# Kernel optimization log

Measured on AMD Instinct MI355X. Metric: run time of the kernel, lower is better.

The kernel has to match this reference:

```python
import jax, jax.numpy as jnp
import numpy as np

EPS = 1e-6
T = 10.0
STEPS = 3
BN_EPS = 1e-5

def _normalize(x, axis):
    n = jnp.sqrt(jnp.sum(x * x, axis=axis, keepdims=True))
    return x / jnp.maximum(n, EPS)

def _vq_step(X, D):
    # X: (B, d, n), D: (B, d, r)
    Dn = _normalize(D, 1)
    Xn = _normalize(X, 1)
    cos = jnp.einsum('bdr,bdn->brn', Dn, Xn)          # (B, r, n)
    C = jax.nn.softmax(cos / T, axis=1)               # softmax over r
    XCt = jnp.einsum('bdn,brn->bdr', X, C)            # (B, d, r)
    sums = jnp.maximum(jnp.sum(C, axis=2), EPS)       # (B, r)
    D2 = _normalize(XCt / sums[:, None, :], 1)
    Xbar = jnp.einsum('bdr,brn->bdn', D2, C)
    return D2, C, Xbar

def _ham_vq(X, D0):
    # K-1 steps without gradient tracking, final step with grad through X only
    Xs = jax.lax.stop_gradient(X)
    def body(D, _):
        D, _, _ = _vq_step(Xs, D)
        return D, None
    D, _ = jax.lax.scan(body, _normalize(D0, 1), None, length=STEPS - 1)
    D = jax.lax.stop_gradient(D)
    _, _, Xbar = _vq_step(X, D)
    return Xbar

def _conv1x1(x, w, b=None):
    y = jnp.einsum('oc,bchw->bohw', w, x)
    if b is not None:
        y = y + b[None, :, None, None]
    return y

def _bn(x, gamma, beta, mean, var):
    inv = gamma / jnp.sqrt(var + BN_EPS)
    return x * inv[None, :, None, None] + (beta - mean * inv)[None, :, None, None]


def setup_inputs() -> dict:
    key = jax.random.key(0)
    ks = jax.random.split(key, 16)
    B, Cin, H, W = 8, 512, 64, 64
    d_mid, r = 512, 64
    out_ch = 2 * d_mid  # dual
    sc = 0.02
    inp = {
        'z': jax.random.normal(ks[0], (B, Cin, H, W), jnp.float32),
        'lower_w': jax.random.normal(ks[1], (out_ch, Cin), jnp.float32) * sc,
        'lower_b': jnp.zeros((out_ch,), jnp.float32),
        'Dinit_s': jax.random.uniform(ks[2], (B, d_mid, r), jnp.float32),
        'Dinit_c': jax.random.uniform(ks[3], (B, d_mid, r), jnp.float32),
        'cheese_w': jax.random.normal(ks[4], (out_ch, out_ch), jnp.float32) * sc,
        'ch_gamma': jnp.ones((out_ch,), jnp.float32),
        'ch_beta': jnp.zeros((out_ch,), jnp.float32),
        'ch_mean': jax.random.normal(ks[5], (out_ch,), jnp.float32) * 0.1,
        'ch_var': jax.random.uniform(ks[6], (out_ch,), jnp.float32) + 0.5,
        'upper_w': jax.random.normal(ks[7], (Cin, out_ch), jnp.float32) * sc,
        'upper_b': jnp.zeros((Cin,), jnp.float32),
        'h_gamma': jnp.ones((Cin,), jnp.float32),
        'h_beta': jnp.zeros((Cin,), jnp.float32),
        'h_mean': jax.random.normal(ks[8], (Cin,), jnp.float32) * 0.1,
        'h_var': jax.random.uniform(ks[9], (Cin,), jnp.float32) + 0.5,
        'coef_ham': jnp.array(1.0, jnp.float32),
        'coef_shortcut': jnp.array(1.0, jnp.float32),
    }
    return inp


def reference(z, lower_w, lower_b, Dinit_s, Dinit_c, cheese_w,
              ch_gamma, ch_beta, ch_mean, ch_var, upper_w, upper_b,
              h_gamma, h_beta, h_mean, h_var, coef_ham, coef_shortcut):
    B, Cin, H, W = z.shape
    identity = z
    # lower: conv1x1 + relu
    y = jax.nn.relu(_conv1x1(z, lower_w, lower_b))       # (B, 2*d_mid, H, W)
    d_mid = y.shape[1] // 2
    y1, y2 = y[:, :d_mid], y[:, d_mid:]
    n = H * W
    # spatial ham
    Xs = y1.reshape(B, d_mid, n)
    y1 = _ham_vq(Xs, Dinit_s).reshape(B, d_mid, H, W)
    # channel ham (same (B, d, n) flattening; HamMD requires dim1 == d_mid)
    Xc = y2.reshape(B, d_mid, n)
    y2 = _ham_vq(Xc, Dinit_c).reshape(B, d_mid, H, W)
    y = jnp.concatenate([y1, y2], axis=1)
    # cheese: conv1x1(no bias) + BN + relu
    y = jax.nn.relu(_bn(_conv1x1(y, cheese_w), ch_gamma, ch_beta, ch_mean, ch_var))
    # upper conv1x1 + BN
    h = _bn(_conv1x1(y, upper_w, upper_b), h_gamma, h_beta, h_mean, h_var)
    out = coef_ham * h + coef_shortcut * identity
    return jax.nn.relu(out)
```

## Files before the change

### kernel.cpp

```cpp
#include <hip/hip_runtime.h>
#include <hip/hip_bf16.h>

typedef __bf16 bf16_t;
typedef __bf16 bf16x4 __attribute__((ext_vector_type(4)));
typedef __bf16 bf16x8 __attribute__((ext_vector_type(8)));
typedef float  f32x4  __attribute__((ext_vector_type(4)));

#define HEPS 1e-6f

__device__ __forceinline__ void gload16(const bf16_t* g, bf16_t* l) {
    __builtin_amdgcn_global_load_lds(
        (const __attribute__((address_space(1))) unsigned int*)(g),
        (__attribute__((address_space(3))) unsigned int*)(l),
        16, 0, 0);
}

__global__ void setup_k(const float* __restrict__ wl, bf16_t* __restrict__ dwl,
                        const float* __restrict__ wc, bf16_t* __restrict__ dwc,
                        const float* __restrict__ wu, bf16_t* __restrict__ dwu,
                        const float* __restrict__ Ds, const float* __restrict__ Dc,
                        bf16_t* __restrict__ Dt,
                        const float* __restrict__ chg, const float* __restrict__ chb,
                        const float* __restrict__ chm, const float* __restrict__ chv,
                        const float* __restrict__ hg, const float* __restrict__ hb,
                        const float* __restrict__ hm, const float* __restrict__ hv,
                        const float* __restrict__ ub, const float* __restrict__ cham,
                        float* __restrict__ chA, float* __restrict__ chB,
                        float* __restrict__ hA2, float* __restrict__ hB2) {
    int bid = blockIdx.x;
    int tid = threadIdx.x;
    if (bid < 8192) {
        int i = bid * 256 + tid;
        if (i < 524288) dwl[i] = (bf16_t)wl[i];
        else if (i < 1572864) { int k = i - 524288; dwc[k] = (bf16_t)wc[k]; }
        else { int k = i - 1572864; dwu[k] = (bf16_t)wu[k]; }
    } else if (bid < 10240) {
        int b2 = bid - 8192;
        int bs = b2 >> 7;
        int idx = (b2 & 127) * 256 + tid;
        int b = bs >> 1;
        const float* src = ((bs & 1) ? Dc : Ds) + (size_t)b * 512 * 64;
        int r = idx & 63, d = idx >> 6;
        Dt[(size_t)bs * 64 * 512 + (size_t)r * 512 + d] = (bf16_t)src[d * 64 + r];
    } else {
        int i = (bid - 10240) * 256 + tid;
        if (i < 1024) {
            float inv = chg[i] * rsqrtf(chv[i] + 1e-5f);
            chA[i] = inv;
            chB[i] = chb[i] - chm[i] * inv;
        }
        if (i < 512) {
            float inv = hg[i] * rsqrtf(hv[i] + 1e-5f);
            float cA = cham[0];
            hA2[i] = cA * inv;
            hB2[i] = cA * (fmaf(ub[i], inv, hb[i]) - hm[i] * inv);
        }
    }
}

__global__ void tz_k(const float* __restrict__ z, bf16_t* __restrict__ Zt,
                     bf16_t* __restrict__ zb) {
    __shared__ bf16_t t[64][68];
    int b = blockIdx.z, kt = blockIdx.y, nt = blockIdx.x;
    const size_t boff = ((size_t)b * 512 + kt * 64) * 4096 + nt * 64;
    const float* src = z + boff;
    bf16_t* zbo = zb + boff;
    int tid = threadIdx.x;
    int kr = tid >> 4;
    int nc = (tid & 15) * 4;
    #pragma unroll
    for (int it = 0; it < 4; ++it) {
        int k = kr + it * 16;
        float4 v = *(const float4*)&src[(size_t)k * 4096 + nc];
        bf16x4 o;
        o[0] = (bf16_t)v.x; o[1] = (bf16_t)v.y; o[2] = (bf16_t)v.z; o[3] = (bf16_t)v.w;
        t[nc + 0][k] = o[0]; t[nc + 1][k] = o[1];
        t[nc + 2][k] = o[2]; t[nc + 3][k] = o[3];
        *(bf16x4*)&zbo[(size_t)k * 4096 + nc] = o;
    }
    __syncthreads();
    bf16_t* dst = Zt + ((size_t)b * 4096 + nt * 64) * 512 + kt * 64;
    int nr = tid >> 4;
    int kc = (tid & 15) * 4;
    #pragma unroll
    for (int it = 0; it < 4; ++it) {
        int n = nr + it * 16;
        bf16x4 o;
        #pragma unroll
        for (int c = 0; c < 4; ++c) o[c] = t[n][kc + c];
        *(bf16x4*)&dst[(size_t)n * 512 + kc] = o;
    }
}

__global__ void dnorm_k(const bf16_t* __restrict__ Dt, float* __restrict__ dinv) {
    int gw = (blockIdx.x * 256 + threadIdx.x) >> 6;
    int lane = threadIdx.x & 63;
    bf16x8 v = *(const bf16x8*)(Dt + (size_t)gw * 512 + lane * 8);
    float s = 0.f;
    #pragma unroll
    for (int e = 0; e < 8; ++e) { float f = (float)v[e]; s += f * f; }
    #pragma unroll
    for (int off = 32; off > 0; off >>= 1) s += __shfl_xor(s, off);
    if (lane == 0) dinv[gw] = 1.0f / fmaxf(sqrtf(s), HEPS);
}

__global__ void reduce_k(const float* __restrict__ P, bf16_t* __restrict__ Dt,
                         float* __restrict__ dinv) {
    int bsr = blockIdx.x;
    int bs = bsr >> 6, r = bsr & 63;
    int lane = threadIdx.x;
    const float* base = P + ((size_t)(bs * 8) * 64 + r) * 512 + lane * 8;
    float s[8] = {0.f, 0.f, 0.f, 0.f, 0.f, 0.f, 0.f, 0.f};
    #pragma unroll
    for (int kc = 0; kc < 8; ++kc) {
        const float* p = base + (size_t)kc * 64 * 512;
        float4 u = *(const float4*)p;
        float4 w = *(const float4*)(p + 4);
        s[0] += u.x; s[1] += u.y; s[2] += u.z; s[3] += u.w;
        s[4] += w.x; s[5] += w.y; s[6] += w.z; s[7] += w.w;
    }
    bf16x8 o;
    float sq = 0.f;
    #pragma unroll
    for (int e = 0; e < 8; ++e) { sq += s[e] * s[e]; o[e] = (bf16_t)s[e]; }
    *(bf16x8*)&Dt[(size_t)bsr * 512 + lane * 8] = o;
    #pragma unroll
    for (int off = 32; off > 0; off >>= 1) sq += __shfl_xor(sq, off);
    if (lane == 0) dinv[bsr] = 1.0f / fmaxf(sqrtf(sq), HEPS);
}

template<int BM, int BN, int WAVES_M, int WAVES_N, int EPI, int ORDER>
__launch_bounds__(256)
__global__ void g2(const bf16_t* __restrict__ Ag, const bf16_t* __restrict__ Bg,
                   void* __restrict__ Cg, void* __restrict__ C2g,
                   const int M, const int N, const int K,
                   const int ldA, const int ldB, const int ldC,
                   const long aStride, const long bStride,
                   const long cStride, const long c2Stride,
                   const float* __restrict__ p0, const float* __restrict__ p1,
                   const float* __restrict__ scal,
                   const void* __restrict__ shortcut, const long sStride)
{
    constexpr int WM = BM / WAVES_M, WN = BN / WAVES_N;
    constexpr int FM = WM / 16, FN = WN / 16;
    constexpr int ASEG = BM / 64, BSEG = BN / 64;
    constexpr int LPT = ASEG + BSEG;

    __shared__ __align__(64) bf16_t SH[3 * (BM + BN) * 32];
    __shared__ float dl[64];
    bf16_t* Al = SH;
    bf16_t* Bl = SH + 3 * BM * 32;

    const int tid = threadIdx.x;
    const int wave = tid >> 6, lane = tid & 63;
    const int l15 = lane & 15, q = lane >> 4;
    const int lrow = lane >> 2, lcol = (lane & 3) * 8;

    const int gx = gridDim.x, gy = gridDim.y;
    const int per = gx * gy;
    const int nwg = per * gridDim.z;
    const int g = blockIdx.z * per + blockIdx.y * gx + blockIdx.x;
    const int qq = nwg >> 3, rr = nwg & 7;
    const int xcd = g & 7, jj = g >> 3;
    const int w = (xcd < rr ? xcd * (qq + 1) : rr * (qq + 1) + (xcd - rr) * qq) + jj;
    const int bz = w / per;
    const int rem = w - bz * per;
    int bx, by;
    if constexpr (ORDER == 0) { by = rem / gx; bx = rem - by * gx; }
    else                      { bx = rem / gy; by = rem - bx * gy; }

    int bs = bz, exA = 0, exB = 0;
    if constexpr (EPI == 5) { bs = bz >> 3; exA = exB = (bz & 7) * 512; }
    if constexpr (EPI == 7) { exA = (bz & 1) * 512; }

    const int n0 = bx * BN;
    const int m0 = by * BM;
    const int wm0 = (wave / WAVES_N) * WM;
    const int wn0 = (wave % WAVES_N) * WN;

    const bf16_t* Ab;
    const bf16_t* Bb;
    if constexpr (EPI == 6) {
        Ab = Ag + (size_t)(bz >> 1) * (size_t)aStride + (size_t)(bz & 1) * 512;
        Bb = Bg + (size_t)bz * (size_t)bStride;
    } else {
        Ab = Ag + (size_t)bs * (size_t)aStride + exA;
        Bb = Bg + (size_t)bs * (size_t)bStride + exB;
    }

    if constexpr (EPI == 6) { if (tid < 64) dl[tid] = p0[bz * 64 + tid]; }

    auto stage = [&](int buf, int k0) {
        #pragma unroll
        for (int t = 0; t < ASEG; ++t) {
            int seg = wave * ASEG + t;
            gload16(Ab + (size_t)(m0 + seg * 16 + lrow) * ldA + k0 + lcol,
                    &Al[buf * BM * 32 + seg * 512]);
        }
        #pragma unroll
        for (int t = 0; t < BSEG; ++t) {
            int seg = wave * BSEG + t;
            gload16(Bb + (size_t)(n0 + seg * 16 + lrow) * ldB + k0 + lcol,
                    &Bl[buf * BN * 32 + seg * 512]);
        }
    };

    f32x4 acc[FM][FN];
    #pragma unroll
    for (int i = 0; i < FM; ++i)
        #pragma unroll
        for (int j = 0; j < FN; ++j)
            #pragma unroll
            for (int e = 0; e < 4; ++e) acc[i][j][e] = 0.f;

    float xsq[FM];
    #pragma unroll
    for (int i = 0; i < FM; ++i) xsq[i] = 0.f;

    const int nK = K / 32;
    stage(0, 0);
    if (nK > 1) stage(1, 32);

    for (int t = 0; t < nK; ++t) {
        const int cur = t % 3;

        if (t < nK - 1) asm volatile("s_waitcnt vmcnt(%0)" :: "i"(LPT) : "memory");
        else            asm volatile("s_waitcnt vmcnt(0)" ::: "memory");
        asm volatile("s_barrier" ::: "memory");
        __builtin_amdgcn_sched_barrier(0);

        if (t + 2 < nK) stage((t + 2) % 3, (t + 2) * 32);

        bf16x8 af[FM], bfm[FN];
        #pragma unroll
        for (int i = 0; i < FM; ++i)
            af[i] = *(const bf16x8*)&Al[cur * BM * 32 + (wm0 + 16 * i + l15) * 32 + 8 * q];
        #pragma unroll
        for (int j = 0; j < FN; ++j)
            bfm[j] = *(const bf16x8*)&Bl[cur * BN * 32 + (wn0 + 16 * j + l15) * 32 + 8 * q];

        if constexpr (EPI == 6) {
            #pragma unroll
            for (int i = 0; i < FM; ++i)
                #pragma unroll
                for (int e = 0; e < 8; ++e) {
                    float f = (float)af[i][e];
                    xsq[i] = fmaf(f, f, xsq[i]);
                }
        }

        __builtin_amdgcn_s_setprio(1);
        #pragma unroll
        for (int i = 0; i < FM; ++i)
            #pragma unroll
            for (int j = 0; j < FN; ++j)
                acc[i][j] = __builtin_amdgcn_mfma_f32_16x16x32_bf16(af[i], bfm[j], acc[i][j], 0, 0, 0);
        __builtin_amdgcn_s_setprio(0);
    }

    int rowB[FM];
    #pragma unroll
    for (int i = 0; i < FM; ++i) rowB[i] = m0 + wm0 + 16 * i + 4 * q;
    const int colBase = n0 + wn0;

    if constexpr (EPI == 2) {
        bf16_t* O = (bf16_t*)Cg + (size_t)bz * (size_t)cStride;
        #pragma unroll
        for (int j = 0; j < FN; ++j) {
            int col = colBase + 16 * j + l15;
            float a = p0[col], b = p1[col];
            #pragma unroll
            for (int i = 0; i < FM; ++i) {
                int rb = rowB[i];
                #pragma unroll
                for (int e = 0; e < 4; ++e) {
                    float v = fmaxf(fmaf(acc[i][j][e], a, b), 0.f);
                    O[(size_t)(rb + e) * ldC + col] = (bf16_t)v;
                }
            }
        }
    } else if constexpr (EPI == 3) {
        constexpr int SPAD = BN + 4;
        constexpr int V = (BM * BN) / 2048;
        float* O = (float*)Cg + (size_t)bz * (size_t)cStride;
        const bf16_t* scg = (const bf16_t*)shortcut + (size_t)bz * (size_t)sStride;
        bf16_t* SP = SH;
        float cB = scal[0];
        __syncthreads();
        #pragma unroll
        for (int v = 0; v < V; ++v) {
            int flat = (tid * V + v) * 8;
            int row = flat / BN, col = flat % BN;
            *(bf16x8*)&SP[row * SPAD + col] =
                *(const bf16x8*)&scg[(size_t)(m0 + row) * ldC + n0 + col];
        }
        __syncthreads();
        #pragma unroll
        for (int i = 0; i < FM; ++i) {
            int rl = wm0 + 16 * i + 4 * q;
            #pragma unroll
            for (int e = 0; e < 4; ++e) {
                int row = m0 + rl + e;
                float a = p0[row], b = p1[row];
                #pragma unroll
                for (int j = 0; j < FN; ++j) {
                    int cl = wn0 + 16 * j + l15;
                    float v = fmaf(acc[i][j][e], a, b)
                            + cB * (float)SP[(rl + e) * SPAD + cl];
                    O[(size_t)row * ldC + n0 + cl] = fmaxf(v, 0.f);
                }
            }
        }
    } else if constexpr (EPI == 5) {
        float* O = (float*)Cg + (size_t)bz * (size_t)cStride;
        #pragma unroll
        for (int i = 0; i < FM; ++i) {
            int rb = rowB[i];
            #pragma unroll
            for (int j = 0; j < FN; ++j) {
                int col = colBase + 16 * j + l15;
                *(f32x4*)&O[(size_t)col * ldC + rb] = acc[i][j];
            }
        }
    } else if constexpr (EPI == 6) {
        bf16_t* Cc = (bf16_t*)Cg  + (size_t)bz * (size_t)cStride;
        bf16_t* Ct = (bf16_t*)C2g + (size_t)(bz >> 1) * (size_t)c2Stride;
        const int hoff = (bz & 1) * 64;
        const bool doCt = (C2g != nullptr);
        float xs[FM];
        #pragma unroll
        for (int i = 0; i < FM; ++i) {
            float s2 = xsq[i];
            s2 += __shfl_xor(s2, 16);
            s2 += __shfl_xor(s2, 32);
            xs[i] = s2;
        }
        float di[FN];
        #pragma unroll
        for (int j = 0; j < FN; ++j) di[j] = dl[16 * j + l15];
        #pragma unroll
        for (int i = 0; i < FM; ++i) {
            int rb = rowB[i];
            bf16x4 tj[FN];
            #pragma unroll
            for (int e = 0; e < 4; ++e) {
                float s2row = __shfl(xs[i], 4 * q + e);
                float xi = 1.0f / (10.0f * fmaxf(sqrtf(s2row), HEPS));
                float v[FN];
                float mx = -1e30f;
                #pragma unroll
                for (int j = 0; j < FN; ++j) {
                    v[j] = acc[i][j][e] * di[j] * xi;
                    mx = fmaxf(mx, v[j]);
                }
                mx = fmaxf(mx, __shfl_xor(mx, 1));
                mx = fmaxf(mx, __shfl_xor(mx, 2));
                mx = fmaxf(mx, __shfl_xor(mx, 4));
                mx = fmaxf(mx, __shfl_xor(mx, 8));
                float sm = 0.f;
                #pragma unroll
                for (int j = 0; j < FN; ++j) { v[j] = __expf(v[j] - mx); sm += v[j]; }
                sm += __shfl_xor(sm, 1);
                sm += __shfl_xor(sm, 2);
                sm += __shfl_xor(sm, 4);
                sm += __shfl_xor(sm, 8);
                float rs = 1.0f / sm;
                #pragma unroll
                for (int j = 0; j < FN; ++j) {
                    float p = v[j] * rs;
                    tj[j][e] = (bf16_t)p;
                    if (doCt) Ct[(size_t)(rb + e) * 128 + hoff + 16 * j + l15] = (bf16_t)p;
                }
            }
            #pragma unroll
            for (int j = 0; j < FN; ++j)
                *(bf16x4*)&Cc[(size_t)(16 * j + l15) * ldC + rb] = tj[j];
        }
    } else if constexpr (EPI == 7) {
        bf16_t* O = (bf16_t*)Cg + (size_t)(bz >> 1) * (size_t)cStride;
        const int hoff = (bz & 1) * 64;
        #pragma unroll
        for (int j = 0; j < FN; ++j) {
            int col = colBase + 16 * j + l15;
            float di = p0[bz * 64 + col];
            #pragma unroll
            for (int i = 0; i < FM; ++i) {
                int rb = rowB[i];
                #pragma unroll
                for (int e = 0; e < 4; ++e)
                    O[(size_t)(rb + e) * 128 + hoff + col] = (bf16_t)(acc[i][j][e] * di);
            }
        }
    } else if constexpr (EPI == 8) {
        bf16_t* O  = (bf16_t*)Cg  + (size_t)bz * (size_t)cStride;
        bf16_t* O2 = (bf16_t*)C2g + (size_t)bz * (size_t)c2Stride;
        #pragma unroll
        for (int j = 0; j < FN; ++j) {
            int col = colBase + 16 * j + l15;
            float bias = p0[col];
            #pragma unroll
            for (int i = 0; i < FM; ++i) {
                int rb = rowB[i];
                bf16x4 t;
                #pragma unroll
                for (int e = 0; e < 4; ++e) {
                    float v = fmaxf(acc[i][j][e] + bias, 0.f);
                    t[e] = (bf16_t)v;
                    O[(size_t)(rb + e) * ldC + col] = t[e];
                }
                *(bf16x4*)&O2[(size_t)col * 4096 + rb] = t;
            }
        }
    }
}


extern "C" void kernel_launch(void* const* d_in, const int* in_sizes, int n_in,
                              void* d_out, int out_size, void* d_ws, size_t ws_size,
                              hipStream_t stream) {
    const float* z        = (const float*)d_in[0];
    const float* lower_w  = (const float*)d_in[1];
    const float* lower_b  = (const float*)d_in[2];
    const float* Dinit_s  = (const float*)d_in[3];
    const float* Dinit_c  = (const float*)d_in[4];
    const float* cheese_w = (const float*)d_in[5];
    const float* ch_gamma = (const float*)d_in[6];
    const float* ch_beta  = (const float*)d_in[7];
    const float* ch_mean  = (const float*)d_in[8];
    const float* ch_var   = (const float*)d_in[9];
    const float* upper_w  = (const float*)d_in[10];
    const float* upper_b  = (const float*)d_in[11];
    const float* h_gamma  = (const float*)d_in[12];
    const float* h_beta   = (const float*)d_in[13];
    const float* h_mean   = (const float*)d_in[14];
    const float* h_var    = (const float*)d_in[15];
    const float* coef_ham = (const float*)d_in[16];
    const float* coef_sc  = (const float*)d_in[17];

    char* ws = (char*)d_ws;
    size_t off = 0;
    auto alloc = [&](size_t bytes) -> void* {
        void* p = ws + off;
        off += (bytes + 255) & ~(size_t)255;
        return p;
    };

    bf16_t* Wl   = (bf16_t*)alloc((size_t)1024 * 512 * 2);
    bf16_t* Wc   = (bf16_t*)alloc((size_t)1024 * 1024 * 2);
    bf16_t* Wu   = (bf16_t*)alloc((size_t)512 * 1024 * 2);
    float*  chA  = (float*) alloc(1024 * 4);
    float*  chB  = (float*) alloc(1024 * 4);
    float*  hA2  = (float*) alloc(512 * 4);
    float*  hB2  = (float*) alloc(512 * 4);
    float*  dinv = (float*) alloc(1024 * 4);
    bf16_t* Xbf  = (bf16_t*)alloc((size_t)8 * 1024 * 4096 * 2);
    bf16_t* Xt   = (bf16_t*)alloc((size_t)8 * 4096 * 1024 * 2);
    bf16_t* Zt   = (bf16_t*)alloc((size_t)8 * 4096 * 512 * 2);
    bf16_t* zb   = (bf16_t*)alloc((size_t)8 * 512 * 4096 * 2);
    bf16_t* Cb   = (bf16_t*)alloc((size_t)16 * 64 * 4096 * 2);
    bf16_t* Ct2  = (bf16_t*)alloc((size_t)8 * 4096 * 128 * 2);
    float*  P    = (float*) alloc((size_t)128 * 64 * 512 * 4);
    bf16_t* Dta  = (bf16_t*)alloc((size_t)16 * 64 * 512 * 2);
    bf16_t* Dtb  = (bf16_t*)alloc((size_t)16 * 64 * 512 * 2);
    bf16_t* Eb   = (bf16_t*)alloc((size_t)8 * 1024 * 128 * 2);
    bf16_t* Ycht = Xbf;

    dim3 blk(256);

    setup_k<<<10244, blk, 0, stream>>>(lower_w, Wl, cheese_w, Wc, upper_w, Wu,
                                       Dinit_s, Dinit_c, Dta,
                                       ch_gamma, ch_beta, ch_mean, ch_var,
                                       h_gamma, h_beta, h_mean, h_var,
                                       upper_b, coef_ham, chA, chB, hA2, hB2);
    tz_k<<<dim3(64, 8, 8), blk, 0, stream>>>(z, Zt, zb);

    g2<128, 64, 2, 2, 8, 0><<<dim3(16, 32, 8), blk, 0, stream>>>(
        Zt, Wl, (void*)Xt, (void*)Xbf, 4096, 1024, 512,
        512, 512, 1024,
        (long)4096 * 512, 0L, (long)4096 * 1024, (long)1024 * 4096,
        lower_b, nullptr, nullptr, nullptr, 0L);

    dnorm_k<<<256, blk, 0, stream>>>(Dta, dinv);

    bf16_t* cur = Dta;
    bf16_t* nxt = Dtb;
    for (int t = 0; t < 3; ++t) {
        g2<128, 64, 4, 1, 6, 0><<<dim3(1, 32, 16), blk, 0, stream>>>(
            Xt, cur, (void*)Cb, (t == 2) ? (void*)Ct2 : nullptr, 4096, 64, 512,
            1024, 512, 4096,
            (long)4096 * 1024, (long)64 * 512, (long)64 * 4096, (long)4096 * 128,
            dinv, nullptr, nullptr, nullptr, 0L);
        g2<64, 64, 2, 2, 5, 0><<<dim3(1, 8, 128), blk, 0, stream>>>(
            Xbf, Cb, (void*)P, nullptr, 512, 64, 512,
            4096, 4096, 512,
            (long)512 * 4096, (long)64 * 4096, (long)64 * 512, 0L,
            nullptr, nullptr, nullptr, nullptr, 0L);
        reduce_k<<<1024, dim3(64), 0, stream>>>(P, nxt, dinv);
        bf16_t* tmp = cur; cur = nxt; nxt = tmp;
    }

    g2<128, 64, 2, 2, 7, 0><<<dim3(1, 8, 16), blk, 0, stream>>>(
        Wc, cur, (void*)Eb, nullptr, 1024, 64, 512,
        1024, 512, 128,
        0L, (long)64 * 512, (long)1024 * 128, 0L,
        dinv, nullptr, nullptr, nullptr, 0L);

    g2<128, 64, 2, 2, 2, 0><<<dim3(16, 32, 8), blk, 0, stream>>>(
        Ct2, Eb, (void*)Ycht, nullptr, 4096, 1024, 128,
        128, 128, 1024,
        (long)4096 * 128, (long)1024 * 128, (long)4096 * 1024, 0L,
        chA, chB, nullptr, nullptr, 0L);

    g2<128, 64, 2, 2, 3, 1><<<dim3(64, 4, 8), blk, 0, stream>>>(
        Wu, Ycht, d_out, nullptr, 512, 4096, 1024,
        1024, 1024, 4096,
        0L, (long)4096 * 1024, (long)512 * 4096, 0L,
        hA2, hB2, coef_sc, zb, (long)512 * 4096);

    (void)in_sizes; (void)n_in; (void)out_size; (void)ws_size;
}
```

Measured before the change: 328.5 us.

## Use 128x128 GEMM tiles, swap lower-conv operands, add separate transpose kernel

Grows the BN tile from 64 to 128 for the lower, cheese and upper 1x1-conv GEMMs to get more reuse per block. The lower conv now computes the transposed product (weights times Zt) with a new epilogue that writes a single layout. A dedicated LDS-tiled transpose kernel then builds the second layout. This replaces the old epilogue's strided scalar dual writes, at the cost of an extra kernel launch and another pass over the activation buffer. The shortcut staging in the final epilogue is rewritten with a hardcoded 128-column pitch to match.

After: 332.5 us. Within noise of the previous version (+1.2%).

```diff
diff --git a/kernel.cpp b/kernel.cpp
--- a/kernel.cpp
+++ b/kernel.cpp
@@ -92,6 +92,30 @@
     }
 }
 
+__global__ void xp_k(const bf16_t* __restrict__ Xt, bf16_t* __restrict__ X) {
+    __shared__ bf16_t t[64][72];
+    int b = blockIdx.z, dt = blockIdx.y, nt = blockIdx.x;
+    const bf16_t* src = Xt + ((size_t)b * 4096 + nt * 64) * 1024 + dt * 64;
+    int tid = threadIdx.x;
+    int r = tid >> 2, c = (tid & 3) * 16;
+    #pragma unroll
+    for (int u = 0; u < 2; ++u) {
+        bf16x8 v = *(const bf16x8*)&src[(size_t)r * 1024 + c + u * 8];
+        *(bf16x8*)&t[r][c + u * 8] = v;
+    }
+    __syncthreads();
+    bf16_t* dst = X + ((size_t)b * 1024 + dt * 64) * 4096 + nt * 64;
+    #pragma unroll
+    for (int u = 0; u < 2; ++u) {
+        int dr = r;
+        int ncol = c + u * 8;
+        bf16x8 o;
+        #pragma unroll
+        for (int e = 0; e < 8; ++e) o[e] = t[ncol + e][dr];
+        *(bf16x8*)&dst[(size_t)dr * 4096 + ncol] = o;
+    }
+}
+
 __global__ void dnorm_k(const bf16_t* __restrict__ Dt, float* __restrict__ dinv) {
     int gw = (blockIdx.x * 256 + threadIdx.x) >> 6;
     int lane = threadIdx.x & 63;
@@ -280,19 +304,17 @@
             }
         }
     } else if constexpr (EPI == 3) {
-        constexpr int SPAD = BN + 4;
-        constexpr int V = (BM * BN) / 2048;
         float* O = (float*)Cg + (size_t)bz * (size_t)cStride;
         const bf16_t* scg = (const bf16_t*)shortcut + (size_t)bz * (size_t)sStride;
         bf16_t* SP = SH;
         float cB = scal[0];
         __syncthreads();
-        #pragma unroll
-        for (int v = 0; v < V; ++v) {
-            int flat = (tid * V + v) * 8;
-            int row = flat / BN, col = flat % BN;
-            *(bf16x8*)&SP[row * SPAD + col] =
-                *(const bf16x8*)&scg[(size_t)(m0 + row) * ldC + n0 + col];
+        {
+            int row = tid >> 1, h = tid & 1;
+            #pragma unroll
+            for (int u = 0; u < 8; ++u)
+                *(bf16x8*)&SP[row * 132 + h * 64 + u * 8] =
+                    *(const bf16x8*)&scg[(size_t)(m0 + row) * ldC + n0 + h * 64 + u * 8];
         }
         __syncthreads();
         #pragma unroll
@@ -306,7 +328,7 @@
                 for (int j = 0; j < FN; ++j) {
                     int cl = wn0 + 16 * j + l15;
                     float v = fmaf(acc[i][j][e], a, b)
-                            + cB * (float)SP[(rl + e) * SPAD + cl];
+                            + cB * (float)SP[(rl + e) * 132 + cl];
                     O[(size_t)row * ldC + n0 + cl] = fmaxf(v, 0.f);
                 }
             }
@@ -391,24 +413,19 @@
                     O[(size_t)(rb + e) * 128 + hoff + col] = (bf16_t)(acc[i][j][e] * di);
             }
         }
-    } else if constexpr (EPI == 8) {
-        bf16_t* O  = (bf16_t*)Cg  + (size_t)bz * (size_t)cStride;
-        bf16_t* O2 = (bf16_t*)C2g + (size_t)bz * (size_t)c2Stride;
+    } else if constexpr (EPI == 9) {
+        bf16_t* O = (bf16_t*)Cg + (size_t)bz * (size_t)cStride;
         #pragma unroll
         for (int j = 0; j < FN; ++j) {
             int col = colBase + 16 * j + l15;
-            float bias = p0[col];
             #pragma unroll
             for (int i = 0; i < FM; ++i) {
                 int rb = rowB[i];
                 bf16x4 t;
                 #pragma unroll
-                for (int e = 0; e < 4; ++e) {
-                    float v = fmaxf(acc[i][j][e] + bias, 0.f);
-                    t[e] = (bf16_t)v;
-                    O[(size_t)(rb + e) * ldC + col] = t[e];
-                }
-                *(bf16x4*)&O2[(size_t)col * 4096 + rb] = t;
+                for (int e = 0; e < 4; ++e)
+                    t[e] = (bf16_t)fmaxf(acc[i][j][e] + p0[rb + e], 0.f);
+                *(bf16x4*)&O[(size_t)col * ldC + rb] = t;
             }
         }
     }
@@ -474,11 +491,13 @@
                                        upper_b, coef_ham, chA, chB, hA2, hB2);
     tz_k<<<dim3(64, 8, 8), blk, 0, stream>>>(z, Zt, zb);
 
-    g2<128, 64, 2, 2, 8, 0><<<dim3(16, 32, 8), blk, 0, stream>>>(
-        Zt, Wl, (void*)Xt, (void*)Xbf, 4096, 1024, 512,
+    g2<128, 128, 2, 2, 9, 0><<<dim3(32, 8, 8), blk, 0, stream>>>(
+        Wl, Zt, (void*)Xt, nullptr, 1024, 4096, 512,
         512, 512, 1024,
-        (long)4096 * 512, 0L, (long)4096 * 1024, (long)1024 * 4096,
+        0L, (long)4096 * 512, (long)4096 * 1024, 0L,
         lower_b, nullptr, nullptr, nullptr, 0L);
+
+    xp_k<<<dim3(64, 16, 8), blk, 0, stream>>>(Xt, Xbf);
 
     dnorm_k<<<256, blk, 0, stream>>>(Dta, dinv);
 
@@ -505,13 +524,13 @@
         0L, (long)64 * 512, (long)1024 * 128, 0L,
         dinv, nullptr, nullptr, nullptr, 0L);
 
-    g2<128, 64, 2, 2, 2, 0><<<dim3(16, 32, 8), blk, 0, stream>>>(
+    g2<128, 128, 2, 2, 2, 0><<<dim3(8, 32, 8), blk, 0, stream>>>(
         Ct2, Eb, (void*)Ycht, nullptr, 4096, 1024, 128,
         128, 128, 1024,
         (long)4096 * 128, (long)1024 * 128, (long)4096 * 1024, 0L,
         chA, chB, nullptr, nullptr, 0L);
 
-    g2<128, 64, 2, 2, 3, 1><<<dim3(64, 4, 8), blk, 0, stream>>>(
+    g2<128, 128, 2, 2, 3, 1><<<dim3(32, 4, 8), blk, 0, stream>>>(
         Wu, Ycht, d_out, nullptr, 512, 4096, 1024,
         1024, 1024, 4096,
         0L, (long)4096 * 1024, (long)512 * 4096, 0L,
```
